# Optimization experiments

Measured on AMD Instinct MI355X. Metric: run time of the kernel, lower is better.

Reference implementation:

```python
import jax, jax.numpy as jnp
import numpy as np

B, D = 65536, 1024
H1, H2, OUT = 512, 256, 12
EPS = 1e-5


def setup_inputs() -> dict:
    key = jax.random.key(0)
    ks = jax.random.split(key, 8)
    x = jax.random.normal(ks[0], (B, D), dtype=jnp.float32)
    W1 = jax.random.normal(ks[1], (D, H1), dtype=jnp.float32) * (1.0 / np.sqrt(D))
    b1 = jnp.zeros((H1,), jnp.float32)
    g1 = jnp.ones((H1,), jnp.float32)
    be1 = jnp.zeros((H1,), jnp.float32)
    W2 = jax.random.normal(ks[2], (H1, H2), dtype=jnp.float32) * (1.0 / np.sqrt(H1))
    b2 = jnp.zeros((H2,), jnp.float32)
    g2 = jnp.ones((H2,), jnp.float32)
    be2 = jnp.zeros((H2,), jnp.float32)
    W3 = jax.random.normal(ks[3], (H2, OUT), dtype=jnp.float32) * (1.0 / np.sqrt(H2))
    b3 = jnp.zeros((OUT,), jnp.float32)
    return {"x": x, "W1": W1, "b1": b1, "g1": g1, "be1": be1,
            "W2": W2, "b2": b2, "g2": g2, "be2": be2, "W3": W3, "b3": b3}


def _bn(h, g, b):
    # BatchNorm1d in training mode: batch mean/var (biased), eps=1e-5
    mu = h.mean(axis=0)
    var = h.var(axis=0)
    return (h - mu) * jax.lax.rsqrt(var + EPS) * g + b


def reference(x, W1, b1, g1, be1, W2, b2, g2, be2, W3, b3):
    h = jax.nn.relu(_bn(x @ W1 + b1, g1, be1))
    h = jax.nn.relu(_bn(h @ W2 + b2, g2, be2))
    y = h @ W3 + b3                      # [B, 12]
    t = y[:, 9:].reshape(-1, 3, 1)       # translation [B,3,1]
    m = y[:, :9].reshape(-1, 3, 3)       # raw rotation [B,3,3]
    # symmetric orthogonalization (SVD-based projection onto SO(3))
    u, s, vt = jnp.linalg.svd(m, full_matrices=False)
    det = jnp.linalg.det(u @ vt)[:, None, None]
    vt_adj = jnp.concatenate([vt[:, :2, :], vt[:, 2:, :] * det], axis=1)
    r = u @ vt_adj                        # [B,3,3], det = +1
    return jnp.concatenate([r, t], axis=-1)  # [B,3,4]
```

## Files before the change

kernel.cpp:

```cpp
#include <hip/hip_runtime.h>

#define B_ROWS 65536
#define D_IN   1024
#define H1N    512
#define H2N    256

typedef _Float16 half8  __attribute__((ext_vector_type(8)));
typedef __fp16   fp16x2 __attribute__((ext_vector_type(2)));
typedef float    f32x4v __attribute__((ext_vector_type(4)));

#define GLOAD_LDS16(gp, lp) \
    __builtin_amdgcn_global_load_lds((const __attribute__((address_space(1))) void*)(gp), \
                                     (__attribute__((address_space(3))) void*)(lp), 16, 0, 0)

__global__ __launch_bounds__(256)
void splitw_t(const float* __restrict__ W, _Float16* __restrict__ wh,
              _Float16* __restrict__ wl, int Kd, int Nd)
{
    __shared__ float tile[64][65];
    const int t = threadIdx.x;
    const int ntn = Nd >> 6;
    const int k0 = (blockIdx.x / ntn) << 6;
    const int n0 = (blockIdx.x % ntn) << 6;

    {
        int r = t >> 4, c4 = (t & 15) << 2;
        #pragma unroll
        for (int i = 0; i < 4; ++i) {
            float4 v = *(const float4*)(W + (size_t)(k0 + r + i * 16) * Nd + n0 + c4);
            tile[r + i*16][c4+0] = v.x; tile[r + i*16][c4+1] = v.y;
            tile[r + i*16][c4+2] = v.z; tile[r + i*16][c4+3] = v.w;
        }
    }
    __syncthreads();
    {
        int n = t >> 2, kc = (t & 3) << 4;
        union { fp16x2 h2[8]; half8 h8[2]; } H, L;
        #pragma unroll
        for (int i = 0; i < 8; ++i) {
            float v0 = tile[kc + 2*i][n], v1 = tile[kc + 2*i + 1][n];
            float h0 = __int_as_float(__float_as_int(v0) & 0xFFFFE000);
            float h1 = __int_as_float(__float_as_int(v1) & 0xFFFFE000);
            H.h2[i] = __builtin_amdgcn_cvt_pkrtz(h0, h1);
            L.h2[i] = __builtin_amdgcn_cvt_pkrtz(v0 - h0, v1 - h1);
        }
        _Float16* ph = wh + (size_t)(n0 + n) * Kd + k0 + kc;
        _Float16* pl = wl + (size_t)(n0 + n) * Kd + k0 + kc;
        *(half8*)ph = H.h8[0]; *(half8*)(ph + 8) = H.h8[1];
        *(half8*)pl = L.h8[0]; *(half8*)(pl + 8) = L.h8[1];
    }
}

template<int K, int NB, bool BNRELU>
__global__ __launch_bounds__(512, 2)
void gemm_fused(const float* __restrict__ Ain, const _Float16* __restrict__ Bth,
                const _Float16* __restrict__ Btl, const float* __restrict__ bias,
                const float2* __restrict__ scsh, float* __restrict__ Cout,
                float2* __restrict__ statp)
{
    constexpr int N  = NB * 256;
    constexpr int NS = K / 32;
    __shared__ alignas(16) char smb[131072 + 4096];
    const int AH0 = 0,     AH1 = 16384, AL0 = 32768, AL1 = 49152;
    const int BH0 = 65536, BH1 = 81920, BL0 = 98304, BL1 = 114688;
    float2* scl = (float2*)(smb + 131072);

    const int tid = threadIdx.x;
    const int l = tid & 63;
    const int w = tid >> 6;
    const int wr = w >> 2, wc = w & 3;

    const int bid = blockIdx.x;
    constexpr int CPX = 32 * NB;
    const int L  = (bid & 7) * CPX + (bid >> 3);
    const int mb = L / NB, nb = L % NB;
    const int m0 = mb << 8, n0 = nb << 8;

    const int ar = tid >> 1, ch = tid & 1;

    if constexpr (BNRELU) {
        for (int i = tid; i < K; i += 512) scl[i] = scsh[i];
    }
    (void)scsh;

    float4 rga[4];
    auto load_regs = [&](int ks) {
        const float4* p = (const float4*)(Ain + (size_t)(m0 + ar) * K + ks * 32 + ch * 16);
        rga[0] = p[0]; rga[1] = p[1]; rga[2] = p[2]; rga[3] = p[3];
    };

    auto stageB = [&](int buf, int ks) {
        #pragma unroll
        for (int i = 0; i < 2; ++i) {
            int rbase = (w * 2 + i) * 16;
            int r = rbase + (l >> 2);
            int c = (l & 3) ^ ((r >> 1) & 3);
            const _Float16* gh = Bth + (size_t)(n0 + r) * K + ks * 32 + c * 8;
            const _Float16* gl = Btl + (size_t)(n0 + r) * K + ks * 32 + c * 8;
            GLOAD_LDS16(gh, smb + (buf ? BH1 : BH0) + rbase * 64);
            GLOAD_LDS16(gl, smb + (buf ? BL1 : BL0) + rbase * 64);
        }
    };

    auto proc_write = [&](int buf, int ks) {
        float v[16];
        #pragma unroll
        for (int p = 0; p < 4; ++p) {
            v[p*4+0] = rga[p].x; v[p*4+1] = rga[p].y;
            v[p*4+2] = rga[p].z; v[p*4+3] = rga[p].w;
        }
        if constexpr (BNRELU) {
            const float2* sp = scl + ks * 32 + ch * 16;
            #pragma unroll
            for (int i = 0; i < 16; ++i) {
                float2 s2 = sp[i];
                v[i] = fmaxf(fmaf(v[i], s2.x, s2.y), 0.f);
            }
        }
        union { fp16x2 h2[4]; half8 h8; } H[2], Lo[2];
        #pragma unroll
        for (int hb = 0; hb < 2; ++hb) {
            #pragma unroll
            for (int i = 0; i < 4; ++i) {
                float v0 = v[hb*8 + 2*i], v1 = v[hb*8 + 2*i + 1];
                float h0 = __int_as_float(__float_as_int(v0) & 0xFFFFE000);
                float h1 = __int_as_float(__float_as_int(v1) & 0xFFFFE000);
                H[hb].h2[i]  = __builtin_amdgcn_cvt_pkrtz(h0, h1);
                Lo[hb].h2[i] = __builtin_amdgcn_cvt_pkrtz(v0 - h0, v1 - h1);
            }
        }
        char* bhp = smb + (buf ? AH1 : AH0) + ar * 64;
        char* blp = smb + (buf ? AL1 : AL0) + ar * 64;
        int sw = (ar >> 1) & 3;
        *(half8*)(bhp + (((ch*2)     ^ sw) * 16)) = H[0].h8;
        *(half8*)(bhp + (((ch*2 + 1) ^ sw) * 16)) = H[1].h8;
        *(half8*)(blp + (((ch*2)     ^ sw) * 16)) = Lo[0].h8;
        *(half8*)(blp + (((ch*2 + 1) ^ sw) * 16)) = Lo[1].h8;
    };

    load_regs(0);
    stageB(0, 0);
    __syncthreads();
    proc_write(0, 0);
    __syncthreads();

    f32x4v acc[8][4] = {};
    for (int ks = 0; ks < NS; ++ks) {
        const int buf = ks & 1;
        if (ks < NS - 1) { load_regs(ks + 1); stageB(buf ^ 1, ks + 1); }

        const char* pah = smb + (buf ? AH1 : AH0);
        const char* pal = smb + (buf ? AL1 : AL0);
        const char* pbh = smb + (buf ? BH1 : BH0);
        const char* pbl = smb + (buf ? BL1 : BL0);

        half8 bh[4], bl[4];
        #pragma unroll
        for (int n = 0; n < 4; ++n) {
            int r = wc * 64 + n * 16 + (l & 15);
            int c = (l >> 4) ^ ((r >> 1) & 3);
            bh[n] = *(const half8*)(pbh + r * 64 + c * 16);
            bl[n] = *(const half8*)(pbl + r * 64 + c * 16);
        }
        #pragma unroll
        for (int mh = 0; mh < 2; ++mh) {
            half8 ah[4], al[4];
            #pragma unroll
            for (int mm = 0; mm < 4; ++mm) {
                int r = wr * 128 + (mh * 4 + mm) * 16 + (l & 15);
                int c = (l >> 4) ^ ((r >> 1) & 3);
                ah[mm] = *(const half8*)(pah + r * 64 + c * 16);
                al[mm] = *(const half8*)(pal + r * 64 + c * 16);
            }
            #pragma unroll
            for (int mm = 0; mm < 4; ++mm) {
                #pragma unroll
                for (int n = 0; n < 4; ++n) {
                    f32x4v t = acc[mh * 4 + mm][n];
                    t = __builtin_amdgcn_mfma_f32_16x16x32_f16(ah[mm], bh[n], t, 0, 0, 0);
                    t = __builtin_amdgcn_mfma_f32_16x16x32_f16(ah[mm], bl[n], t, 0, 0, 0);
                    t = __builtin_amdgcn_mfma_f32_16x16x32_f16(al[mm], bh[n], t, 0, 0, 0);
                    acc[mh * 4 + mm][n] = t;
                }
            }
        }
        if (ks < NS - 1) proc_write(buf ^ 1, ks + 1);
        __syncthreads();
    }

    float bv[4], s[4], q[4];
    #pragma unroll
    for (int n = 0; n < 4; ++n) {
        bv[n] = bias[n0 + wc * 64 + n * 16 + (l & 15)];
        s[n] = 0.f; q[n] = 0.f;
    }
    #pragma unroll
    for (int m = 0; m < 8; ++m) {
        int row = m0 + wr * 128 + m * 16 + ((l >> 4) << 2);
        #pragma unroll
        for (int n = 0; n < 4; ++n) {
            int col = n0 + wc * 64 + n * 16 + (l & 15);
            float* cp = Cout + (size_t)row * N + col;
            #pragma unroll
            for (int j = 0; j < 4; ++j) {
                float v = acc[m][n][j] + bv[n];
                cp[(size_t)j * N] = v;
                s[n] += v; q[n] += v * v;
            }
        }
    }
    #pragma unroll
    for (int n = 0; n < 4; ++n) {
        s[n] += __shfl_xor(s[n], 16); s[n] += __shfl_xor(s[n], 32);
        q[n] += __shfl_xor(q[n], 16); q[n] += __shfl_xor(q[n], 32);
    }
    __syncthreads();
    float2* red = (float2*)smb;
    if (wr == 1 && l < 16) {
        #pragma unroll
        for (int n = 0; n < 4; ++n) red[(wc * 4 + n) * 16 + l] = make_float2(s[n], q[n]);
    }
    __syncthreads();
    if (wr == 0 && l < 16) {
        #pragma unroll
        for (int n = 0; n < 4; ++n) {
            float2 o = red[(wc * 4 + n) * 16 + l];
            int col = n0 + wc * 64 + n * 16 + l;
            statp[(size_t)mb * N + col] = make_float2(s[n] + o.x, q[n] + o.y);
        }
    }
}

__global__ void reduce_stats_g(const float2* __restrict__ part, int nparts, int ncols,
                               const float* __restrict__ g, const float* __restrict__ be,
                               float2* __restrict__ scsh)
{
    int c = blockIdx.x * blockDim.x + threadIdx.x;
    if (c >= ncols) return;
    float s = 0.f, q = 0.f;
    for (int p = 0; p < nparts; ++p) {
        float2 v = part[(size_t)p * ncols + c];
        s += v.x; q += v.y;
    }
    const float invB = 1.f / 65536.f;
    float mu = s * invB, var = q * invB - mu * mu;
    float sc = g[c] * rsqrtf(var + 1e-5f);
    scsh[c] = make_float2(sc, be[c] - mu * sc);
}

__device__ __forceinline__ void jrot(float A[3][3], float V[3][3], int p, int q)
{
    float apq = A[p][q];
    float tau = A[q][q] - A[p][p];
    float a2  = 2.f * apq;
    float Dd  = fabsf(tau) + sqrtf(tau * tau + a2 * a2) + 1e-38f;
    float tt  = copysignf(1.f, tau) * a2 / Dd;
    float c   = 1.f / sqrtf(1.f + tt * tt);
    float s   = tt * c;
    int   r   = 3 - p - q;
    float App = A[p][p], Aqq = A[q][q];
    A[p][p] = App - tt * apq;
    A[q][q] = Aqq + tt * apq;
    A[p][q] = 0.f; A[q][p] = 0.f;
    float Arp = A[r][p], Arq = A[r][q];
    A[r][p] = c * Arp - s * Arq; A[p][r] = A[r][p];
    A[r][q] = s * Arp + c * Arq; A[q][r] = A[r][q];
    #pragma unroll
    for (int i = 0; i < 3; ++i) {
        float vp = V[i][p], vq = V[i][q];
        V[i][p] = c * vp - s * vq;
        V[i][q] = s * vp + c * vq;
    }
}

__global__ __launch_bounds__(256)
void head_svd(const float* __restrict__ H2, const float2* __restrict__ scsh2,
              const float* __restrict__ W3, const float* __restrict__ b3,
              float* __restrict__ out)
{
    __shared__ alignas(16) float  w3s[H2N * 12];
    __shared__ alignas(16) float2 ss[H2N];
    __shared__ float b3s[12];
    __shared__ alignas(16) float tile[64][257];

    const int t = threadIdx.x;
    for (int i = t; i < H2N * 12; i += 256) w3s[i] = W3[i];
    ss[t] = scsh2[t];
    if (t < 12) b3s[t] = b3[t];
    __syncthreads();

    const size_t rbase = (size_t)blockIdx.x * 256;
    const size_t row = rbase + t;
    float y[12];
    #pragma unroll
    for (int o = 0; o < 12; ++o) y[o] = b3s[o];

    for (int kc = 0; kc < 4; ++kc) {
        #pragma unroll
        for (int i = 0; i < 16; ++i) {
            int rr = (t >> 4) + i * 16;
            int k4 = (t & 15) * 4;
            float4 v = *(const float4*)(H2 + (rbase + rr) * H2N + kc * 64 + k4);
            float2 sA = ss[kc*64 + k4 + 0];
            float2 sB = ss[kc*64 + k4 + 1];
            float2 sC = ss[kc*64 + k4 + 2];
            float2 sD = ss[kc*64 + k4 + 3];
            tile[k4+0][rr] = fmaxf(fmaf(v.x, sA.x, sA.y), 0.f);
            tile[k4+1][rr] = fmaxf(fmaf(v.y, sB.x, sB.y), 0.f);
            tile[k4+2][rr] = fmaxf(fmaf(v.z, sC.x, sC.y), 0.f);
            tile[k4+3][rr] = fmaxf(fmaf(v.w, sD.x, sD.y), 0.f);
        }
        __syncthreads();
        #pragma unroll 4
        for (int k = 0; k < 64; ++k) {
            float v = tile[k][t];
            const float* wp = &w3s[(kc * 64 + k) * 12];
            #pragma unroll
            for (int o = 0; o < 12; ++o) y[o] = fmaf(v, wp[o], y[o]);
        }
        __syncthreads();
    }

    float mm[3][3];
    #pragma unroll
    for (int i = 0; i < 3; ++i)
        #pragma unroll
        for (int j = 0; j < 3; ++j) mm[i][j] = y[i * 3 + j];

    float Am[3][3];
    #pragma unroll
    for (int i = 0; i < 3; ++i)
        #pragma unroll
        for (int j = 0; j < 3; ++j)
            Am[i][j] = mm[0][i]*mm[0][j] + mm[1][i]*mm[1][j] + mm[2][i]*mm[2][j];

    float V[3][3] = {{1,0,0},{0,1,0},{0,0,1}};
    #pragma unroll
    for (int sweep = 0; sweep < 5; ++sweep) {
        jrot(Am, V, 0, 1);
        jrot(Am, V, 0, 2);
        jrot(Am, V, 1, 2);
    }
    float lam0 = Am[0][0], lam1 = Am[1][1], lam2 = Am[2][2];
    if (lam0 < lam1) { float tl=lam0; lam0=lam1; lam1=tl;
        #pragma unroll
        for (int i=0;i<3;++i){float tv=V[i][0];V[i][0]=V[i][1];V[i][1]=tv;} }
    if (lam0 < lam2) { float tl=lam0; lam0=lam2; lam2=tl;
        #pragma unroll
        for (int i=0;i<3;++i){float tv=V[i][0];V[i][0]=V[i][2];V[i][2]=tv;} }
    if (lam1 < lam2) { float tl=lam1; lam1=lam2; lam2=tl;
        #pragma unroll
        for (int i=0;i<3;++i){float tv=V[i][1];V[i][1]=V[i][2];V[i][2]=tv;} }

    float det =
          V[0][0]*(V[1][1]*V[2][2]-V[1][2]*V[2][1])
        - V[0][1]*(V[1][0]*V[2][2]-V[1][2]*V[2][0])
        + V[0][2]*(V[1][0]*V[2][1]-V[1][1]*V[2][0]);
    if (det < 0.f) { V[0][2] = -V[0][2]; V[1][2] = -V[1][2]; V[2][2] = -V[2][2]; }

    float u0[3], u1[3], u2[3];
    #pragma unroll
    for (int i = 0; i < 3; ++i)
        u0[i] = mm[i][0]*V[0][0] + mm[i][1]*V[1][0] + mm[i][2]*V[2][0];
    float nn0 = 1.f / sqrtf(u0[0]*u0[0] + u0[1]*u0[1] + u0[2]*u0[2] + 1e-30f);
    u0[0]*=nn0; u0[1]*=nn0; u0[2]*=nn0;
    #pragma unroll
    for (int i = 0; i < 3; ++i)
        u1[i] = mm[i][0]*V[0][1] + mm[i][1]*V[1][1] + mm[i][2]*V[2][1];
    float d01 = u0[0]*u1[0] + u0[1]*u1[1] + u0[2]*u1[2];
    u1[0]-=d01*u0[0]; u1[1]-=d01*u0[1]; u1[2]-=d01*u0[2];
    float nn1 = 1.f / sqrtf(u1[0]*u1[0] + u1[1]*u1[1] + u1[2]*u1[2] + 1e-30f);
    u1[0]*=nn1; u1[1]*=nn1; u1[2]*=nn1;
    u2[0] = u0[1]*u1[2] - u0[2]*u1[1];
    u2[1] = u0[2]*u1[0] - u0[0]*u1[2];
    u2[2] = u0[0]*u1[1] - u0[1]*u1[0];

    float* op = out + row * 12;
    #pragma unroll
    for (int i = 0; i < 3; ++i) {
        #pragma unroll
        for (int j = 0; j < 3; ++j)
            op[i*4 + j] = u0[i]*V[j][0] + u1[i]*V[j][1] + u2[i]*V[j][2];
        op[i*4 + 3] = y[9 + i];
    }
}

extern "C" void kernel_launch(void* const* d_in, const int* in_sizes, int n_in,
                              void* d_out, int out_size, void* d_ws, size_t ws_size,
                              hipStream_t stream)
{
    (void)in_sizes; (void)n_in; (void)out_size; (void)ws_size;

    const float* x   = (const float*)d_in[0];
    const float* W1  = (const float*)d_in[1];
    const float* b1  = (const float*)d_in[2];
    const float* g1  = (const float*)d_in[3];
    const float* be1 = (const float*)d_in[4];
    const float* W2  = (const float*)d_in[5];
    const float* b2  = (const float*)d_in[6];
    const float* g2  = (const float*)d_in[7];
    const float* be2 = (const float*)d_in[8];
    const float* W3  = (const float*)d_in[9];
    const float* b3  = (const float*)d_in[10];
    float* out = (float*)d_out;

    char* ws = (char*)d_ws;
    size_t off = 0;
    auto take = [&](size_t bytes) -> void* {
        void* p = ws + off;
        off += (bytes + 255) & ~(size_t)255;
        return p;
    };
    _Float16* w1h = (_Float16*)take((size_t)H1N * D_IN * 2);
    _Float16* w1l = (_Float16*)take((size_t)H1N * D_IN * 2);
    _Float16* w2h = (_Float16*)take((size_t)H2N * H1N * 2);
    _Float16* w2l = (_Float16*)take((size_t)H2N * H1N * 2);
    float*  h1    = (float*) take((size_t)B_ROWS * H1N * 4);
    float*  h2    = (float*) take((size_t)B_ROWS * H2N * 4);
    float2* part1 = (float2*)take((size_t)256 * H1N * 8);
    float2* part2 = (float2*)take((size_t)256 * H2N * 8);
    float2* scsh1 = (float2*)take((size_t)H1N * 8);
    float2* scsh2 = (float2*)take((size_t)H2N * 8);

    splitw_t<<<dim3((D_IN/64) * (H1N/64)), dim3(256), 0, stream>>>(W1, w1h, w1l, D_IN, H1N);
    splitw_t<<<dim3((H1N/64) * (H2N/64)), dim3(256), 0, stream>>>(W2, w2h, w2l, H1N, H2N);

    gemm_fused<D_IN, 2, false><<<dim3(512), dim3(512), 0, stream>>>(
        x, w1h, w1l, b1, nullptr, h1, part1);
    reduce_stats_g<<<dim3(2), dim3(256), 0, stream>>>(part1, 256, H1N, g1, be1, scsh1);

    gemm_fused<H1N, 1, true><<<dim3(256), dim3(512), 0, stream>>>(
        h1, w2h, w2l, b2, scsh1, h2, part2);
    reduce_stats_g<<<dim3(1), dim3(256), 0, stream>>>(part2, 256, H2N, g2, be2, scsh2);

    head_svd<<<dim3(B_ROWS / 256), dim3(256), 0, stream>>>(h2, scsh2, W3, b3, out);
}
```

Baseline: 411.5 us.

## Stage fp32 A tiles directly to LDS and split fp16 hi/lo at read time

The A operand is now copied as fp32 straight from global memory into swizzled LDS with async global_load_lds, replacing the register round-trip and separate convert-and-write step. The BN/ReLU and hi/lo fp16 split run when fragments are read from LDS. The main loop is unrolled by two with explicit ping-pong buffers, raw s_barrier calls, vmcnt waits and s_setprio around the MFMA bursts, so loads overlap compute. The cost is redundant conversion work, because every wave re-splits the A fragments it reads. The hand-placed barriers also risk hazards and assume an even number of K steps.

```diff
diff --git a/kernel.cpp b/kernel.cpp
--- a/kernel.cpp
+++ b/kernel.cpp
@@ -60,9 +60,11 @@
 {
     constexpr int N  = NB * 256;
     constexpr int NS = K / 32;
+    constexpr int NI = NS / 2;
     __shared__ alignas(16) char smb[131072 + 4096];
-    const int AH0 = 0,     AH1 = 16384, AL0 = 32768, AL1 = 49152;
-    const int BH0 = 65536, BH1 = 81920, BL0 = 98304, BL1 = 114688;
+    const int A0 = 0,      A1  = 32768;
+    const int BH0 = 65536, BH1 = 81920;
+    const int BL0 = 98304, BL1 = 114688;
     float2* scl = (float2*)(smb + 131072);
 
     const int tid = threadIdx.x;
@@ -76,20 +78,15 @@
     const int mb = L / NB, nb = L % NB;
     const int m0 = mb << 8, n0 = nb << 8;
 
-    const int ar = tid >> 1, ch = tid & 1;
-
-    if constexpr (BNRELU) {
-        for (int i = tid; i < K; i += 512) scl[i] = scsh[i];
-    }
-    (void)scsh;
-
-    float4 rga[4];
-    auto load_regs = [&](int ks) {
-        const float4* p = (const float4*)(Ain + (size_t)(m0 + ar) * K + ks * 32 + ch * 16);
-        rga[0] = p[0]; rga[1] = p[1]; rga[2] = p[2]; rga[3] = p[3];
-    };
-
-    auto stageB = [&](int buf, int ks) {
+    auto stageAll = [&](int ks, int offA, int offBH, int offBL) {
+        #pragma unroll
+        for (int i = 0; i < 4; ++i) {
+            int rbase = w * 32 + i * 8;
+            int r = rbase + (l >> 3);
+            int c = (l & 7) ^ (r & 7);
+            const float* g = Ain + (size_t)(m0 + r) * K + ks * 32 + c * 4;
+            GLOAD_LDS16(g, smb + offA + rbase * 128);
+        }
         #pragma unroll
         for (int i = 0; i < 2; ++i) {
             int rbase = (w * 2 + i) * 16;
@@ -97,95 +94,113 @@
             int c = (l & 3) ^ ((r >> 1) & 3);
             const _Float16* gh = Bth + (size_t)(n0 + r) * K + ks * 32 + c * 8;
             const _Float16* gl = Btl + (size_t)(n0 + r) * K + ks * 32 + c * 8;
-            GLOAD_LDS16(gh, smb + (buf ? BH1 : BH0) + rbase * 64);
-            GLOAD_LDS16(gl, smb + (buf ? BL1 : BL0) + rbase * 64);
-        }
-    };
-
-    auto proc_write = [&](int buf, int ks) {
-        float v[16];
-        #pragma unroll
-        for (int p = 0; p < 4; ++p) {
-            v[p*4+0] = rga[p].x; v[p*4+1] = rga[p].y;
-            v[p*4+2] = rga[p].z; v[p*4+3] = rga[p].w;
-        }
+            GLOAD_LDS16(gh, smb + offBH + rbase * 64);
+            GLOAD_LDS16(gl, smb + offBL + rbase * 64);
+        }
+    };
+
+    half8 bh[4], bl[4], ah[4], al[4];
+    float2 ssreg[8];
+    f32x4v acc[8][4] = {};
+
+    auto loadss = [&](int ks) {
         if constexpr (BNRELU) {
-            const float2* sp = scl + ks * 32 + ch * 16;
+            const float2* sp = scl + ks * 32 + ((l >> 4) << 3);
             #pragma unroll
-            for (int i = 0; i < 16; ++i) {
-                float2 s2 = sp[i];
-                v[i] = fmaxf(fmaf(v[i], s2.x, s2.y), 0.f);
-            }
-        }
-        union { fp16x2 h2[4]; half8 h8; } H[2], Lo[2];
-        #pragma unroll
-        for (int hb = 0; hb < 2; ++hb) {
-            #pragma unroll
-            for (int i = 0; i < 4; ++i) {
-                float v0 = v[hb*8 + 2*i], v1 = v[hb*8 + 2*i + 1];
-                float h0 = __int_as_float(__float_as_int(v0) & 0xFFFFE000);
-                float h1 = __int_as_float(__float_as_int(v1) & 0xFFFFE000);
-                H[hb].h2[i]  = __builtin_amdgcn_cvt_pkrtz(h0, h1);
-                Lo[hb].h2[i] = __builtin_amdgcn_cvt_pkrtz(v0 - h0, v1 - h1);
-            }
-        }
-        char* bhp = smb + (buf ? AH1 : AH0) + ar * 64;
-        char* blp = smb + (buf ? AL1 : AL0) + ar * 64;
-        int sw = (ar >> 1) & 3;
-        *(half8*)(bhp + (((ch*2)     ^ sw) * 16)) = H[0].h8;
-        *(half8*)(bhp + (((ch*2 + 1) ^ sw) * 16)) = H[1].h8;
-        *(half8*)(blp + (((ch*2)     ^ sw) * 16)) = Lo[0].h8;
-        *(half8*)(blp + (((ch*2 + 1) ^ sw) * 16)) = Lo[1].h8;
-    };
-
-    load_regs(0);
-    stageB(0, 0);
-    __syncthreads();
-    proc_write(0, 0);
-    __syncthreads();
-
-    f32x4v acc[8][4] = {};
-    for (int ks = 0; ks < NS; ++ks) {
-        const int buf = ks & 1;
-        if (ks < NS - 1) { load_regs(ks + 1); stageB(buf ^ 1, ks + 1); }
-
-        const char* pah = smb + (buf ? AH1 : AH0);
-        const char* pal = smb + (buf ? AL1 : AL0);
-        const char* pbh = smb + (buf ? BH1 : BH0);
-        const char* pbl = smb + (buf ? BL1 : BL0);
-
-        half8 bh[4], bl[4];
+            for (int i = 0; i < 8; ++i) ssreg[i] = sp[i];
+        }
+        (void)ks;
+    };
+
+    auto dsreadB = [&](int offBH, int offBL) {
         #pragma unroll
         for (int n = 0; n < 4; ++n) {
             int r = wc * 64 + n * 16 + (l & 15);
             int c = (l >> 4) ^ ((r >> 1) & 3);
-            bh[n] = *(const half8*)(pbh + r * 64 + c * 16);
-            bl[n] = *(const half8*)(pbl + r * 64 + c * 16);
-        }
-        #pragma unroll
-        for (int mh = 0; mh < 2; ++mh) {
-            half8 ah[4], al[4];
-            #pragma unroll
-            for (int mm = 0; mm < 4; ++mm) {
-                int r = wr * 128 + (mh * 4 + mm) * 16 + (l & 15);
-                int c = (l >> 4) ^ ((r >> 1) & 3);
-                ah[mm] = *(const half8*)(pah + r * 64 + c * 16);
-                al[mm] = *(const half8*)(pal + r * 64 + c * 16);
-            }
-            #pragma unroll
-            for (int mm = 0; mm < 4; ++mm) {
+            bh[n] = *(const half8*)(smb + offBH + r * 64 + c * 16);
+            bl[n] = *(const half8*)(smb + offBL + r * 64 + c * 16);
+        }
+    };
+
+    auto dsreadA = [&](int offA, int mh) {
+        #pragma unroll
+        for (int mm = 0; mm < 4; ++mm) {
+            int r = wr * 128 + (mh * 4 + mm) * 16 + (l & 15);
+            const char* base = smb + offA + r * 128;
+            int c0 = ((l >> 4) * 2) ^ (r & 7);
+            int c1 = (((l >> 4) * 2) | 1) ^ (r & 7);
+            f32x4v va = *(const f32x4v*)(base + c0 * 16);
+            f32x4v vb = *(const f32x4v*)(base + c1 * 16);
+            if constexpr (BNRELU) {
                 #pragma unroll
-                for (int n = 0; n < 4; ++n) {
-                    f32x4v t = acc[mh * 4 + mm][n];
-                    t = __builtin_amdgcn_mfma_f32_16x16x32_f16(ah[mm], bh[n], t, 0, 0, 0);
-                    t = __builtin_amdgcn_mfma_f32_16x16x32_f16(ah[mm], bl[n], t, 0, 0, 0);
-                    t = __builtin_amdgcn_mfma_f32_16x16x32_f16(al[mm], bh[n], t, 0, 0, 0);
-                    acc[mh * 4 + mm][n] = t;
+                for (int e = 0; e < 4; ++e) {
+                    va[e] = fmaxf(fmaf(va[e], ssreg[e].x,     ssreg[e].y),     0.f);
+                    vb[e] = fmaxf(fmaf(vb[e], ssreg[4 + e].x, ssreg[4 + e].y), 0.f);
                 }
             }
-        }
-        if (ks < NS - 1) proc_write(buf ^ 1, ks + 1);
-        __syncthreads();
+            union { fp16x2 h2[4]; half8 h8; } H, Lo;
+            #pragma unroll
+            for (int i = 0; i < 4; ++i) {
+                float a0 = (i < 2) ? va[2*i] : vb[2*(i-2)];
+                float a1 = (i < 2) ? va[2*i+1] : vb[2*(i-2)+1];
+                float h0 = __int_as_float(__float_as_int(a0) & 0xFFFFE000);
+                float h1 = __int_as_float(__float_as_int(a1) & 0xFFFFE000);
+                H.h2[i]  = __builtin_amdgcn_cvt_pkrtz(h0, h1);
+                Lo.h2[i] = __builtin_amdgcn_cvt_pkrtz(a0 - h0, a1 - h1);
+            }
+            ah[mm] = H.h8; al[mm] = Lo.h8;
+        }
+    };
+
+    auto mfma48 = [&](int mh) {
+        __builtin_amdgcn_s_setprio(1);
+        #pragma unroll
+        for (int mm = 0; mm < 4; ++mm) {
+            #pragma unroll
+            for (int n = 0; n < 4; ++n) {
+                f32x4v t = acc[mh * 4 + mm][n];
+                t = __builtin_amdgcn_mfma_f32_16x16x32_f16(ah[mm], bh[n], t, 0, 0, 0);
+                t = __builtin_amdgcn_mfma_f32_16x16x32_f16(ah[mm], bl[n], t, 0, 0, 0);
+                t = __builtin_amdgcn_mfma_f32_16x16x32_f16(al[mm], bh[n], t, 0, 0, 0);
+                acc[mh * 4 + mm][n] = t;
+            }
+        }
+        __builtin_amdgcn_s_setprio(0);
+    };
+
+    if constexpr (BNRELU) {
+        for (int i = tid; i < K; i += 512) scl[i] = scsh[i];
+    }
+    (void)scsh;
+    stageAll(0, A0, BH0, BL0);
+    __syncthreads();
+
+    for (int j = 0; j < NI; ++j) {
+        const int sa = 2 * j, sb = 2 * j + 1;
+        loadss(sa);
+        dsreadB(BH0, BL0);
+        dsreadA(A0, 0);
+        stageAll(sb, A1, BH1, BL1);
+        __builtin_amdgcn_s_barrier();
+        mfma48(0);
+        __builtin_amdgcn_s_barrier();
+        dsreadA(A0, 1);
+        __builtin_amdgcn_s_barrier();
+        mfma48(1);
+        asm volatile("s_waitcnt vmcnt(0)" ::: "memory");
+        __builtin_amdgcn_s_barrier();
+        loadss(sb);
+        dsreadB(BH1, BL1);
+        dsreadA(A1, 0);
+        if (j < NI - 1) stageAll(sa + 2, A0, BH0, BL0);
+        __builtin_amdgcn_s_barrier();
+        mfma48(0);
+        __builtin_amdgcn_s_barrier();
+        dsreadA(A1, 1);
+        __builtin_amdgcn_s_barrier();
+        mfma48(1);
+        asm volatile("s_waitcnt vmcnt(0)" ::: "memory");
+        __builtin_amdgcn_s_barrier();
     }
 
     float bv[4], s[4], q[4];
```

Result: slower. 539.1 us (+31.0%).

## Replace LDS-staged GEMM with direct-to-register MFMA-fragment loads

Applied to the files above, without the earlier changes.

Weights are pre-split into fp16 hi/lo and written in MFMA-fragment order, so each lane can load its B fragments straight from global memory. The GEMM no longer stages A and B through shared memory or double-buffers, and it drops the per-step __syncthreads. Tiles shrink to 128x256 with 256-thread blocks, which doubles the block count and the stat partials. The cost is that A rows are read uncoalesced from global memory and B fragments are re-read by every block through cache, with no LDS reuse.

```diff
diff --git a/kernel.cpp b/kernel.cpp
--- a/kernel.cpp
+++ b/kernel.cpp
@@ -9,19 +9,15 @@
 typedef __fp16   fp16x2 __attribute__((ext_vector_type(2)));
 typedef float    f32x4v __attribute__((ext_vector_type(4)));
 
-#define GLOAD_LDS16(gp, lp) \
-    __builtin_amdgcn_global_load_lds((const __attribute__((address_space(1))) void*)(gp), \
-                                     (__attribute__((address_space(3))) void*)(lp), 16, 0, 0)
-
 __global__ __launch_bounds__(256)
-void splitw_t(const float* __restrict__ W, _Float16* __restrict__ wh,
-              _Float16* __restrict__ wl, int Kd, int Nd)
+void splitw_pk(const float* __restrict__ W, half8* __restrict__ ph,
+               half8* __restrict__ pl, int Kd, int Nd)
 {
     __shared__ float tile[64][65];
     const int t = threadIdx.x;
     const int ntn = Nd >> 6;
-    const int k0 = (blockIdx.x / ntn) << 6;
-    const int n0 = (blockIdx.x % ntn) << 6;
+    const int kt = blockIdx.x / ntn, nt = blockIdx.x % ntn;
+    const int k0 = kt << 6, n0 = nt << 6;
 
     {
         int r = t >> 4, c4 = (t & 15) << 2;
@@ -33,173 +29,131 @@
         }
     }
     __syncthreads();
-    {
-        int n = t >> 2, kc = (t & 3) << 4;
-        union { fp16x2 h2[8]; half8 h8[2]; } H, L;
-        #pragma unroll
-        for (int i = 0; i < 8; ++i) {
-            float v0 = tile[kc + 2*i][n], v1 = tile[kc + 2*i + 1][n];
+    #pragma unroll
+    for (int uu = 0; uu < 2; ++uu) {
+        int u = t + uu * 256;
+        int l = u & 63, nfl = (u >> 6) & 3, ksl = u >> 8;
+        int col = nfl * 16 + (l & 15);
+        int kb  = ksl * 32 + (l >> 4) * 8;
+        union { fp16x2 h2[4]; half8 h8; } H, L;
+        #pragma unroll
+        for (int i = 0; i < 4; ++i) {
+            float v0 = tile[kb + 2*i][col], v1 = tile[kb + 2*i + 1][col];
             float h0 = __int_as_float(__float_as_int(v0) & 0xFFFFE000);
             float h1 = __int_as_float(__float_as_int(v1) & 0xFFFFE000);
             H.h2[i] = __builtin_amdgcn_cvt_pkrtz(h0, h1);
             L.h2[i] = __builtin_amdgcn_cvt_pkrtz(v0 - h0, v1 - h1);
         }
-        _Float16* ph = wh + (size_t)(n0 + n) * Kd + k0 + kc;
-        _Float16* pl = wl + (size_t)(n0 + n) * Kd + k0 + kc;
-        *(half8*)ph = H.h8[0]; *(half8*)(ph + 8) = H.h8[1];
-        *(half8*)pl = L.h8[0]; *(half8*)(pl + 8) = L.h8[1];
-    }
-}
-
-template<int K, int NB, bool BNRELU>
-__global__ __launch_bounds__(512, 2)
-void gemm_fused(const float* __restrict__ Ain, const _Float16* __restrict__ Bth,
-                const _Float16* __restrict__ Btl, const float* __restrict__ bias,
-                const float2* __restrict__ scsh, float* __restrict__ Cout,
-                float2* __restrict__ statp)
-{
-    constexpr int N  = NB * 256;
+        size_t idx = ((size_t)((kt*2 + ksl) * (Nd >> 4) + nt*4 + nfl)) * 64 + l;
+        ph[idx] = H.h8;
+        pl[idx] = L.h8;
+    }
+}
+
+template<int K, int NBn, bool BNRELU>
+__global__ __launch_bounds__(256, 2)
+void gemm_direct(const float* __restrict__ Ain, const half8* __restrict__ Bph,
+                 const half8* __restrict__ Bpl, const float* __restrict__ bias,
+                 const float2* __restrict__ scsh, float* __restrict__ Cout,
+                 float2* __restrict__ statp)
+{
+    constexpr int N  = NBn * 256;
     constexpr int NS = K / 32;
-    __shared__ alignas(16) char smb[131072 + 4096];
-    const int AH0 = 0,     AH1 = 16384, AL0 = 32768, AL1 = 49152;
-    const int BH0 = 65536, BH1 = 81920, BL0 = 98304, BL1 = 114688;
-    float2* scl = (float2*)(smb + 131072);
+    constexpr int NF = N / 16;
+    __shared__ float2 scl[BNRELU ? K : 8];
+    __shared__ float2 sred[256];
 
     const int tid = threadIdx.x;
     const int l = tid & 63;
     const int w = tid >> 6;
-    const int wr = w >> 2, wc = w & 3;
-
+    const int wr = w >> 1, wc = w & 1;
+
+    constexpr int NWG = NBn * 512;
     const int bid = blockIdx.x;
-    constexpr int CPX = 32 * NB;
-    const int L  = (bid & 7) * CPX + (bid >> 3);
-    const int mb = L / NB, nb = L % NB;
-    const int m0 = mb << 8, n0 = nb << 8;
-
-    const int ar = tid >> 1, ch = tid & 1;
+    const int L = (bid & 7) * (NWG >> 3) + (bid >> 3);
+    const int mb = L / NBn, nbi = L % NBn;
+    const int m0 = mb << 7, n0 = nbi << 8;
 
     if constexpr (BNRELU) {
-        for (int i = tid; i < K; i += 512) scl[i] = scsh[i];
+        for (int i = tid; i < K; i += 256) scl[i] = scsh[i];
+        __syncthreads();
     }
     (void)scsh;
 
-    float4 rga[4];
-    auto load_regs = [&](int ks) {
-        const float4* p = (const float4*)(Ain + (size_t)(m0 + ar) * K + ks * 32 + ch * 16);
-        rga[0] = p[0]; rga[1] = p[1]; rga[2] = p[2]; rga[3] = p[3];
-    };
-
-    auto stageB = [&](int buf, int ks) {
-        #pragma unroll
-        for (int i = 0; i < 2; ++i) {
-            int rbase = (w * 2 + i) * 16;
-            int r = rbase + (l >> 2);
-            int c = (l & 3) ^ ((r >> 1) & 3);
-            const _Float16* gh = Bth + (size_t)(n0 + r) * K + ks * 32 + c * 8;
-            const _Float16* gl = Btl + (size_t)(n0 + r) * K + ks * 32 + c * 8;
-            GLOAD_LDS16(gh, smb + (buf ? BH1 : BH0) + rbase * 64);
-            GLOAD_LDS16(gl, smb + (buf ? BL1 : BL0) + rbase * 64);
-        }
-    };
-
-    auto proc_write = [&](int buf, int ks) {
-        float v[16];
-        #pragma unroll
-        for (int p = 0; p < 4; ++p) {
-            v[p*4+0] = rga[p].x; v[p*4+1] = rga[p].y;
-            v[p*4+2] = rga[p].z; v[p*4+3] = rga[p].w;
-        }
+    const int kg = l >> 4;
+    const float* aptr = Ain + (size_t)(m0 + wr * 64 + (l & 15)) * K + kg * 8;
+    const int nfb = (n0 >> 4) + wc * 8;
+
+    f32x4v acc[4][8] = {};
+
+    #pragma unroll 2
+    for (int ks = 0; ks < NS; ++ks) {
+        float2 ss[8];
         if constexpr (BNRELU) {
-            const float2* sp = scl + ks * 32 + ch * 16;
-            #pragma unroll
-            for (int i = 0; i < 16; ++i) {
-                float2 s2 = sp[i];
-                v[i] = fmaxf(fmaf(v[i], s2.x, s2.y), 0.f);
-            }
-        }
-        union { fp16x2 h2[4]; half8 h8; } H[2], Lo[2];
-        #pragma unroll
-        for (int hb = 0; hb < 2; ++hb) {
+            const float2* sp = scl + ks * 32 + kg * 8;
+            #pragma unroll
+            for (int i = 0; i < 8; ++i) ss[i] = sp[i];
+        }
+        half8 ah[4], al[4];
+        #pragma unroll
+        for (int mm = 0; mm < 4; ++mm) {
+            const float* p = aptr + (size_t)mm * 16 * K + ks * 32;
+            f32x4v va = *(const f32x4v*)p;
+            f32x4v vb = *(const f32x4v*)(p + 4);
+            if constexpr (BNRELU) {
+                #pragma unroll
+                for (int e = 0; e < 4; ++e) {
+                    va[e] = fmaxf(fmaf(va[e], ss[e].x,     ss[e].y),     0.f);
+                    vb[e] = fmaxf(fmaf(vb[e], ss[4 + e].x, ss[4 + e].y), 0.f);
+                }
+            }
+            union { fp16x2 h2[4]; half8 h8; } H, Lo;
             #pragma unroll
             for (int i = 0; i < 4; ++i) {
-                float v0 = v[hb*8 + 2*i], v1 = v[hb*8 + 2*i + 1];
-                float h0 = __int_as_float(__float_as_int(v0) & 0xFFFFE000);
-                float h1 = __int_as_float(__float_as_int(v1) & 0xFFFFE000);
-                H[hb].h2[i]  = __builtin_amdgcn_cvt_pkrtz(h0, h1);
-                Lo[hb].h2[i] = __builtin_amdgcn_cvt_pkrtz(v0 - h0, v1 - h1);
-            }
-        }
-        char* bhp = smb + (buf ? AH1 : AH0) + ar * 64;
-        char* blp = smb + (buf ? AL1 : AL0) + ar * 64;
-        int sw = (ar >> 1) & 3;
-        *(half8*)(bhp + (((ch*2)     ^ sw) * 16)) = H[0].h8;
-        *(half8*)(bhp + (((ch*2 + 1) ^ sw) * 16)) = H[1].h8;
-        *(half8*)(blp + (((ch*2)     ^ sw) * 16)) = Lo[0].h8;
-        *(half8*)(blp + (((ch*2 + 1) ^ sw) * 16)) = Lo[1].h8;
-    };
-
-    load_regs(0);
-    stageB(0, 0);
-    __syncthreads();
-    proc_write(0, 0);
-    __syncthreads();
-
-    f32x4v acc[8][4] = {};
-    for (int ks = 0; ks < NS; ++ks) {
-        const int buf = ks & 1;
-        if (ks < NS - 1) { load_regs(ks + 1); stageB(buf ^ 1, ks + 1); }
-
-        const char* pah = smb + (buf ? AH1 : AH0);
-        const char* pal = smb + (buf ? AL1 : AL0);
-        const char* pbh = smb + (buf ? BH1 : BH0);
-        const char* pbl = smb + (buf ? BL1 : BL0);
-
-        half8 bh[4], bl[4];
-        #pragma unroll
-        for (int n = 0; n < 4; ++n) {
-            int r = wc * 64 + n * 16 + (l & 15);
-            int c = (l >> 4) ^ ((r >> 1) & 3);
-            bh[n] = *(const half8*)(pbh + r * 64 + c * 16);
-            bl[n] = *(const half8*)(pbl + r * 64 + c * 16);
-        }
-        #pragma unroll
-        for (int mh = 0; mh < 2; ++mh) {
-            half8 ah[4], al[4];
-            #pragma unroll
-            for (int mm = 0; mm < 4; ++mm) {
-                int r = wr * 128 + (mh * 4 + mm) * 16 + (l & 15);
-                int c = (l >> 4) ^ ((r >> 1) & 3);
-                ah[mm] = *(const half8*)(pah + r * 64 + c * 16);
-                al[mm] = *(const half8*)(pal + r * 64 + c * 16);
+                float a0 = (i < 2) ? va[2*i]     : vb[2*(i-2)];
+                float a1 = (i < 2) ? va[2*i + 1] : vb[2*(i-2) + 1];
+                float h0 = __int_as_float(__float_as_int(a0) & 0xFFFFE000);
+                float h1 = __int_as_float(__float_as_int(a1) & 0xFFFFE000);
+                H.h2[i]  = __builtin_amdgcn_cvt_pkrtz(h0, h1);
+                Lo.h2[i] = __builtin_amdgcn_cvt_pkrtz(a0 - h0, a1 - h1);
+            }
+            ah[mm] = H.h8; al[mm] = Lo.h8;
+        }
+        #pragma unroll
+        for (int nh = 0; nh < 2; ++nh) {
+            half8 bh[4], bl[4];
+            #pragma unroll
+            for (int nf = 0; nf < 4; ++nf) {
+                size_t idx = ((size_t)ks * NF + nfb + nh * 4 + nf) * 64 + l;
+                bh[nf] = Bph[idx];
+                bl[nf] = Bpl[idx];
             }
             #pragma unroll
             for (int mm = 0; mm < 4; ++mm) {
                 #pragma unroll
-                for (int n = 0; n < 4; ++n) {
-                    f32x4v t = acc[mh * 4 + mm][n];
-                    t = __builtin_amdgcn_mfma_f32_16x16x32_f16(ah[mm], bh[n], t, 0, 0, 0);
-                    t = __builtin_amdgcn_mfma_f32_16x16x32_f16(ah[mm], bl[n], t, 0, 0, 0);
-                    t = __builtin_amdgcn_mfma_f32_16x16x32_f16(al[mm], bh[n], t, 0, 0, 0);
-                    acc[mh * 4 + mm][n] = t;
+                for (int nf = 0; nf < 4; ++nf) {
+                    f32x4v t = acc[mm][nh * 4 + nf];
+                    t = __builtin_amdgcn_mfma_f32_16x16x32_f16(ah[mm], bh[nf], t, 0, 0, 0);
+                    t = __builtin_amdgcn_mfma_f32_16x16x32_f16(ah[mm], bl[nf], t, 0, 0, 0);
+                    t = __builtin_amdgcn_mfma_f32_16x16x32_f16(al[mm], bh[nf], t, 0, 0, 0);
+                    acc[mm][nh * 4 + nf] = t;
                 }
             }
         }
-        if (ks < NS - 1) proc_write(buf ^ 1, ks + 1);
-        __syncthreads();
-    }
-
-    float bv[4], s[4], q[4];
-    #pragma unroll
-    for (int n = 0; n < 4; ++n) {
-        bv[n] = bias[n0 + wc * 64 + n * 16 + (l & 15)];
+    }
+
+    float bv[8], s[8], q[8];
+    #pragma unroll
+    for (int n = 0; n < 8; ++n) {
+        bv[n] = bias[n0 + wc * 128 + n * 16 + (l & 15)];
         s[n] = 0.f; q[n] = 0.f;
     }
     #pragma unroll
-    for (int m = 0; m < 8; ++m) {
-        int row = m0 + wr * 128 + m * 16 + ((l >> 4) << 2);
-        #pragma unroll
-        for (int n = 0; n < 4; ++n) {
-            int col = n0 + wc * 64 + n * 16 + (l & 15);
+    for (int m = 0; m < 4; ++m) {
+        int row = m0 + wr * 64 + m * 16 + ((l >> 4) << 2);
+        #pragma unroll
+        for (int n = 0; n < 8; ++n) {
+            int col = n0 + wc * 128 + n * 16 + (l & 15);
             float* cp = Cout + (size_t)row * N + col;
             #pragma unroll
             for (int j = 0; j < 4; ++j) {
@@ -210,22 +164,21 @@
         }
     }
     #pragma unroll
-    for (int n = 0; n < 4; ++n) {
+    for (int n = 0; n < 8; ++n) {
         s[n] += __shfl_xor(s[n], 16); s[n] += __shfl_xor(s[n], 32);
         q[n] += __shfl_xor(q[n], 16); q[n] += __shfl_xor(q[n], 32);
     }
     __syncthreads();
-    float2* red = (float2*)smb;
     if (wr == 1 && l < 16) {
         #pragma unroll
-        for (int n = 0; n < 4; ++n) red[(wc * 4 + n) * 16 + l] = make_float2(s[n], q[n]);
+        for (int n = 0; n < 8; ++n) sred[(wc * 8 + n) * 16 + l] = make_float2(s[n], q[n]);
     }
     __syncthreads();
     if (wr == 0 && l < 16) {
         #pragma unroll
-        for (int n = 0; n < 4; ++n) {
-            float2 o = red[(wc * 4 + n) * 16 + l];
-            int col = n0 + wc * 64 + n * 16 + l;
+        for (int n = 0; n < 8; ++n) {
+            float2 o = sred[(wc * 8 + n) * 16 + l];
+            int col = n0 + wc * 128 + n * 16 + l;
             statp[(size_t)mb * N + col] = make_float2(s[n] + o.x, q[n] + o.y);
         }
     }
@@ -411,27 +364,27 @@
         off += (bytes + 255) & ~(size_t)255;
         return p;
     };
-    _Float16* w1h = (_Float16*)take((size_t)H1N * D_IN * 2);
-    _Float16* w1l = (_Float16*)take((size_t)H1N * D_IN * 2);
-    _Float16* w2h = (_Float16*)take((size_t)H2N * H1N * 2);
-    _Float16* w2l = (_Float16*)take((size_t)H2N * H1N * 2);
+    half8* w1h = (half8*)take((size_t)H1N * D_IN * 2);
+    half8* w1l = (half8*)take((size_t)H1N * D_IN * 2);
+    half8* w2h = (half8*)take((size_t)H2N * H1N * 2);
+    half8* w2l = (half8*)take((size_t)H2N * H1N * 2);
     float*  h1    = (float*) take((size_t)B_ROWS * H1N * 4);
     float*  h2    = (float*) take((size_t)B_ROWS * H2N * 4);
-    float2* part1 = (float2*)take((size_t)256 * H1N * 8);
-    float2* part2 = (float2*)take((size_t)256 * H2N * 8);
+    float2* part1 = (float2*)take((size_t)512 * H1N * 8);
+    float2* part2 = (float2*)take((size_t)512 * H2N * 8);
     float2* scsh1 = (float2*)take((size_t)H1N * 8);
     float2* scsh2 = (float2*)take((size_t)H2N * 8);
 
-    splitw_t<<<dim3((D_IN/64) * (H1N/64)), dim3(256), 0, stream>>>(W1, w1h, w1l, D_IN, H1N);
-    splitw_t<<<dim3((H1N/64) * (H2N/64)), dim3(256), 0, stream>>>(W2, w2h, w2l, H1N, H2N);
-
-    gemm_fused<D_IN, 2, false><<<dim3(512), dim3(512), 0, stream>>>(
+    splitw_pk<<<dim3((D_IN/64) * (H1N/64)), dim3(256), 0, stream>>>(W1, w1h, w1l, D_IN, H1N);
+    splitw_pk<<<dim3((H1N/64) * (H2N/64)), dim3(256), 0, stream>>>(W2, w2h, w2l, H1N, H2N);
+
+    gemm_direct<D_IN, 2, false><<<dim3(1024), dim3(256), 0, stream>>>(
         x, w1h, w1l, b1, nullptr, h1, part1);
-    reduce_stats_g<<<dim3(2), dim3(256), 0, stream>>>(part1, 256, H1N, g1, be1, scsh1);
-
-    gemm_fused<H1N, 1, true><<<dim3(256), dim3(512), 0, stream>>>(
+    reduce_stats_g<<<dim3(2), dim3(256), 0, stream>>>(part1, 512, H1N, g1, be1, scsh1);
+
+    gemm_direct<H1N, 1, true><<<dim3(512), dim3(256), 0, stream>>>(
         h1, w2h, w2l, b2, scsh1, h2, part2);
-    reduce_stats_g<<<dim3(1), dim3(256), 0, stream>>>(part2, 256, H2N, g2, be2, scsh2);
+    reduce_stats_g<<<dim3(1), dim3(256), 0, stream>>>(part2, 512, H2N, g2, be2, scsh2);
 
     head_svd<<<dim3(B_ROWS / 256), dim3(256), 0, stream>>>(h2, scsh2, W3, b3, out);
 }
```

Result: slower. 664.9 us (+61.6%).
